# Performance work log

Hardware: AMD Instinct MI355X
Metric: run time of the kernel (lower is better)

Reference implementation:

```python
import jax, jax.numpy as jnp
import numpy as np

N_BASIS = 32
EMBED_DIM = 256
MAX_STD = 4.0
EPS = 1e-4
B, X, A = 8, 4096, 64


def setup_inputs() -> dict:
    key = jax.random.key(0)
    k1, k2, k3 = jax.random.split(key, 3)
    wrho = jax.random.uniform(k1, (B, X), dtype=jnp.float32)
    distances = jax.random.uniform(k2, (B, X, A), dtype=jnp.float32)
    # buffer: gammas = 1 / (2 * stds^2) with stds = linspace(0, max_std, n_basis+1)[1:]
    stds = jnp.linspace(0.0, MAX_STD, N_BASIS + 1, dtype=jnp.float32)[1:]
    gammas = 1.0 / (2.0 * stds ** 2)
    W = jax.random.normal(k3, (EMBED_DIM, N_BASIS), dtype=jnp.float32) / np.sqrt(N_BASIS)
    return {"wrho": wrho, "distances": distances, "gammas": gammas, "W": W}


def reference(wrho, distances, gammas, W):
    # norms: (s,)  Gaussian normalization constants
    norms = (jnp.pi / gammas) ** 1.5
    # basis_vals: (b, x, a, s) = norms * exp(-gammas * d^2)
    basis_vals = norms * jnp.exp(-gammas * distances[..., None] ** 2)
    # weighted pooling over grid points x -> (b, a, s)
    pooled_rho = jnp.einsum('bxas,bx->bas', basis_vals, wrho)
    phi = jnp.log(pooled_rho + EPS)
    # linear lift (no bias): (b, a, embed_dim)
    return jnp.einsum('bas,es->bae', phi, W)
```

## Files before the change

kernel.cpp:

```cpp
#include <hip/hip_runtime.h>
#include <math.h>

#define NB 32
#define ED 256
#define BB 8
#define XX 4096
#define AA 64
#define EPS 1e-4f
#define LOG2E 1.44269504088896340736f
#define LN2   0.69314718055994530942f
#define PI_F  3.14159265358979323846f

template <int XC>
__global__ __launch_bounds__(256) void k_pool(
    const float* __restrict__ wrho,
    const float* __restrict__ dist,
    const float* __restrict__ gammas,
    float* __restrict__ part)
{
    constexpr int XPB = XX / XC;
    constexpr int XPW = XPB / 4;
    const int blk = blockIdx.x;
    const int b = blk / XC;
    const int c = blk % XC;
    const int t = threadIdx.x;
    const int a = t & 63;
    const int w = t >> 6;

    float mg2[NB];
#pragma unroll
    for (int s = 0; s < NB; ++s) {
        float g = gammas[s];
        float v = -g * LOG2E;
        mg2[s] = __uint_as_float(__builtin_amdgcn_readfirstlane(__float_as_uint(v)));
    }

    float acc[NB];
#pragma unroll
    for (int s = 0; s < NB; ++s) acc[s] = 0.f;

    const int x0 = c * XPB + w * XPW;
    const float* dptr = dist + ((size_t)b * XX + x0) * AA + a;
    const float* wptr = wrho + (size_t)b * XX + x0;

    for (int i = 0; i < XPW; ++i) {
        float d  = dptr[(size_t)i * AA];
        float wv = __uint_as_float(__builtin_amdgcn_readfirstlane(
                       __float_as_uint(wptr[i])));
        float d2 = d * d;
#pragma unroll
        for (int s = 0; s < NB; ++s) {
            float e = exp2f(mg2[s] * d2);
            acc[s] = fmaf(wv, e, acc[s]);
        }
    }

    __shared__ float red[4][AA][NB + 1];
#pragma unroll
    for (int s = 0; s < NB; ++s) red[w][a][s] = acc[s];
    __syncthreads();

    for (int p = t; p < AA * NB; p += 256) {
        int pa = p >> 5, ps = p & 31;
        float v = red[0][pa][ps] + red[1][pa][ps] + red[2][pa][ps] + red[3][pa][ps];
        part[(((size_t)b * AA + pa) * XC + c) * NB + ps] = v;
    }
}

template <int XC>
__global__ __launch_bounds__(256) void k_lift(
    const float* __restrict__ part,
    const float* __restrict__ gammas,
    const float* __restrict__ W,
    float* __restrict__ out)
{
    const int blk = blockIdx.x;
    const int b = blk >> 6;
    const int a = blk & 63;
    const int t = threadIdx.x;

    __shared__ float phi[NB];
    __shared__ float red[8][NB];

    const float* p = part + (((size_t)b * AA + a) * XC) * NB;
    {
        int s = t & 31, g = t >> 5;
        float sum = 0.f;
        for (int c = g; c < XC; c += 8) sum += p[c * NB + s];
        red[g][s] = sum;
    }
    __syncthreads();
    if (t < NB) {
        float sum = 0.f;
#pragma unroll
        for (int g = 0; g < 8; ++g) sum += red[g][t];
        float gm = gammas[t];
        float norm = exp2f(1.5f * log2f(PI_F / gm));
        phi[t] = LN2 * log2f(fmaf(norm, sum, EPS));
    }
    __syncthreads();

    const float4* Wv = (const float4*)(W + (size_t)t * NB);
    float r = 0.f;
#pragma unroll
    for (int q = 0; q < NB / 4; ++q) {
        float4 wv = Wv[q];
        r = fmaf(wv.x, phi[q * 4 + 0], r);
        r = fmaf(wv.y, phi[q * 4 + 1], r);
        r = fmaf(wv.z, phi[q * 4 + 2], r);
        r = fmaf(wv.w, phi[q * 4 + 3], r);
    }
    out[((size_t)b * AA + a) * ED + t] = r;
}

extern "C" void kernel_launch(void* const* d_in, const int* in_sizes, int n_in,
                              void* d_out, int out_size, void* d_ws, size_t ws_size,
                              hipStream_t stream) {
    const float* wrho   = (const float*)d_in[0];
    const float* dist   = (const float*)d_in[1];
    const float* gammas = (const float*)d_in[2];
    const float* W      = (const float*)d_in[3];
    float* out  = (float*)d_out;
    float* part = (float*)d_ws;

    const size_t need64 = (size_t)BB * AA * 64 * NB * sizeof(float);
    const size_t need16 = (size_t)BB * AA * 16 * NB * sizeof(float);

    if (ws_size >= need64) {
        k_pool<64><<<BB * 64, 256, 0, stream>>>(wrho, dist, gammas, part);
        k_lift<64><<<BB * AA, 256, 0, stream>>>(part, gammas, W, out);
    } else if (ws_size >= need16) {
        k_pool<16><<<BB * 16, 256, 0, stream>>>(wrho, dist, gammas, part);
        k_lift<16><<<BB * AA, 256, 0, stream>>>(part, gammas, W, out);
    } else {
        k_pool<4><<<BB * 4, 256, 0, stream>>>(wrho, dist, gammas, part);
        k_lift<4><<<BB * AA, 256, 0, stream>>>(part, gammas, W, out);
    }
}
```

Baseline: 90.46 us.

## Fuse pooling and lift into one kernel with per-basis thread mapping

```diff
diff --git a/kernel.cpp b/kernel.cpp
--- a/kernel.cpp
+++ b/kernel.cpp
@@ -11,89 +11,50 @@
 #define LN2   0.69314718055994530942f
 #define PI_F  3.14159265358979323846f
 
-template <int XC>
-__global__ __launch_bounds__(256) void k_pool(
+__global__ __launch_bounds__(256) void k_fused(
     const float* __restrict__ wrho,
     const float* __restrict__ dist,
-    const float* __restrict__ gammas,
-    float* __restrict__ part)
-{
-    constexpr int XPB = XX / XC;
-    constexpr int XPW = XPB / 4;
-    const int blk = blockIdx.x;
-    const int b = blk / XC;
-    const int c = blk % XC;
-    const int t = threadIdx.x;
-    const int a = t & 63;
-    const int w = t >> 6;
-
-    float mg2[NB];
-#pragma unroll
-    for (int s = 0; s < NB; ++s) {
-        float g = gammas[s];
-        float v = -g * LOG2E;
-        mg2[s] = __uint_as_float(__builtin_amdgcn_readfirstlane(__float_as_uint(v)));
-    }
-
-    float acc[NB];
-#pragma unroll
-    for (int s = 0; s < NB; ++s) acc[s] = 0.f;
-
-    const int x0 = c * XPB + w * XPW;
-    const float* dptr = dist + ((size_t)b * XX + x0) * AA + a;
-    const float* wptr = wrho + (size_t)b * XX + x0;
-
-    for (int i = 0; i < XPW; ++i) {
-        float d  = dptr[(size_t)i * AA];
-        float wv = __uint_as_float(__builtin_amdgcn_readfirstlane(
-                       __float_as_uint(wptr[i])));
-        float d2 = d * d;
-#pragma unroll
-        for (int s = 0; s < NB; ++s) {
-            float e = exp2f(mg2[s] * d2);
-            acc[s] = fmaf(wv, e, acc[s]);
-        }
-    }
-
-    __shared__ float red[4][AA][NB + 1];
-#pragma unroll
-    for (int s = 0; s < NB; ++s) red[w][a][s] = acc[s];
-    __syncthreads();
-
-    for (int p = t; p < AA * NB; p += 256) {
-        int pa = p >> 5, ps = p & 31;
-        float v = red[0][pa][ps] + red[1][pa][ps] + red[2][pa][ps] + red[3][pa][ps];
-        part[(((size_t)b * AA + pa) * XC + c) * NB + ps] = v;
-    }
-}
-
-template <int XC>
-__global__ __launch_bounds__(256) void k_lift(
-    const float* __restrict__ part,
     const float* __restrict__ gammas,
     const float* __restrict__ W,
     float* __restrict__ out)
 {
-    const int blk = blockIdx.x;
-    const int b = blk >> 6;
-    const int a = blk & 63;
+    constexpr int XPT = XX / 8;
+    const int bid = blockIdx.x;
+    const int b = bid >> 6;
+    const int a = bid & 63;
     const int t = threadIdx.x;
+    const int s = t & 31;
+    const int g = t >> 5;
 
+    const float mg = -gammas[s] * LOG2E;
+
+    const int xb = g * XPT;
+    const float* dptr = dist + ((size_t)b * XX + xb) * AA + a;
+    const float* wptr = wrho + (size_t)b * XX + xb;
+
+    float acc = 0.f;
+    for (int i0 = 0; i0 < XPT; i0 += 8) {
+        float4 wA = *(const float4*)(wptr + i0);
+        float4 wB = *(const float4*)(wptr + i0 + 4);
+        float d[8];
+#pragma unroll
+        for (int j = 0; j < 8; ++j) d[j] = dptr[(size_t)(i0 + j) * AA];
+        float wv[8] = {wA.x, wA.y, wA.z, wA.w, wB.x, wB.y, wB.z, wB.w};
+#pragma unroll
+        for (int j = 0; j < 8; ++j) {
+            float e = __builtin_amdgcn_exp2f(mg * (d[j] * d[j]));
+            acc = fmaf(wv[j], e, acc);
+        }
+    }
+
+    __shared__ float red[8][NB + 1];
     __shared__ float phi[NB];
-    __shared__ float red[8][NB];
-
-    const float* p = part + (((size_t)b * AA + a) * XC) * NB;
-    {
-        int s = t & 31, g = t >> 5;
-        float sum = 0.f;
-        for (int c = g; c < XC; c += 8) sum += p[c * NB + s];
-        red[g][s] = sum;
-    }
+    red[g][s] = acc;
     __syncthreads();
     if (t < NB) {
         float sum = 0.f;
 #pragma unroll
-        for (int g = 0; g < 8; ++g) sum += red[g][t];
+        for (int q = 0; q < 8; ++q) sum += red[q][t];
         float gm = gammas[t];
         float norm = exp2f(1.5f * log2f(PI_F / gm));
         phi[t] = LN2 * log2f(fmaf(norm, sum, EPS));
@@ -104,11 +65,11 @@
     float r = 0.f;
 #pragma unroll
     for (int q = 0; q < NB / 4; ++q) {
-        float4 wv = Wv[q];
-        r = fmaf(wv.x, phi[q * 4 + 0], r);
-        r = fmaf(wv.y, phi[q * 4 + 1], r);
-        r = fmaf(wv.z, phi[q * 4 + 2], r);
-        r = fmaf(wv.w, phi[q * 4 + 3], r);
+        float4 w4 = Wv[q];
+        r = fmaf(w4.x, phi[q * 4 + 0], r);
+        r = fmaf(w4.y, phi[q * 4 + 1], r);
+        r = fmaf(w4.z, phi[q * 4 + 2], r);
+        r = fmaf(w4.w, phi[q * 4 + 3], r);
     }
     out[((size_t)b * AA + a) * ED + t] = r;
 }
@@ -120,20 +81,8 @@
     const float* dist   = (const float*)d_in[1];
     const float* gammas = (const float*)d_in[2];
     const float* W      = (const float*)d_in[3];
-    float* out  = (float*)d_out;
-    float* part = (float*)d_ws;
+    float* out = (float*)d_out;
+    (void)d_ws; (void)ws_size; (void)in_sizes; (void)n_in; (void)out_size;
 
-    const size_t need64 = (size_t)BB * AA * 64 * NB * sizeof(float);
-    const size_t need16 = (size_t)BB * AA * 16 * NB * sizeof(float);
-
-    if (ws_size >= need64) {
-        k_pool<64><<<BB * 64, 256, 0, stream>>>(wrho, dist, gammas, part);
-        k_lift<64><<<BB * AA, 256, 0, stream>>>(part, gammas, W, out);
-    } else if (ws_size >= need16) {
-        k_pool<16><<<BB * 16, 256, 0, stream>>>(wrho, dist, gammas, part);
-        k_lift<16><<<BB * AA, 256, 0, stream>>>(part, gammas, W, out);
-    } else {
-        k_pool<4><<<BB * 4, 256, 0, stream>>>(wrho, dist, gammas, part);
-        k_lift<4><<<BB * AA, 256, 0, stream>>>(part, gammas, W, out);
-    }
+    k_fused<<<BB * AA, 256, 0, stream>>>(wrho, dist, gammas, W, out);
 }
```

Result: faster. 83.26 us (-8.0%).
